# Optimization experiments

Measured on AMD Instinct MI355X. Metric: run time of the kernel, lower is better.

## Reference

```python
import jax, jax.numpy as jnp
import numpy as np

B, HOR, E, L = 16, 512, 1024, 12
ACT_NUM, DIM, ADIM = 10, 64, 10
N = 2 * HOR                      # backbone sequence length (test=False)
NPOS = 4 * (1 + HOR)             # wpe table size
D_IN = 3 + DIM * ACT_NUM + ADIM  # embed_transition input dim = 653


def setup_inputs() -> dict:
    key = jax.random.key(0)
    ks = jax.random.split(key, 12)
    s = lambda k, shape: (jax.random.normal(k, shape, jnp.float32) * 0.02)
    return {
        "action_set": jax.random.normal(ks[0], (B, ACT_NUM, DIM), jnp.float32),
        "context_rewards": jax.random.normal(ks[1], (B, HOR, 1), jnp.float32),
        "wpe": s(ks[2], (NPOS, E)),
        "W_emb": s(ks[3], (D_IN, E)),
        "b_emb": jnp.zeros((E,), jnp.float32),
        "Wq": s(ks[4], (L, E, E)),
        "Wk": s(ks[5], (L, E, E)),
        "Wv": s(ks[6], (L, E, E)),
        "ln1_g": jnp.ones((L, E), jnp.float32),
        "ln1_b": jnp.zeros((L, E), jnp.float32),
        "W1": s(ks[7], (L, E, E)),
        "b1": jnp.zeros((L, E), jnp.float32),
        "W2": s(ks[8], (L, E, E)),
        "b2": jnp.zeros((L, E), jnp.float32),
        "ln2_g": jnp.ones((L, E), jnp.float32),
        "ln2_b": jnp.zeros((L, E), jnp.float32),
        "W_pred": s(ks[9], (E, ADIM)),
        "b_pred": jnp.zeros((ADIM,), jnp.float32),
    }


def _layernorm(x, g, b, eps=1e-5):
    mu = x.mean(-1, keepdims=True)
    var = ((x - mu) ** 2).mean(-1, keepdims=True)
    return (x - mu) * jax.lax.rsqrt(var + eps) * g + b


def reference(action_set, context_rewards, wpe, W_emb, b_emb, Wq, Wk, Wv,
              ln1_g, ln1_b, W1, b1, W2, b2, ln2_g, ln2_b, W_pred, b_pred):
    batch = action_set.shape[0]
    hor = context_rewards.shape[1]
    n = 2 * hor
    # --- build interleaved sequence (outer Transformer glue) ---
    a = action_set.reshape(batch, 1, -1)                       # [B,1,DA]
    pair = jnp.concatenate([a, jnp.zeros_like(a)], axis=1)     # [B,2,DA]
    act_set_seq = jnp.tile(pair, (1, hor, 1))                  # [B,2H,DA]
    action_seq = jnp.zeros((batch, n, ADIM + 1), jnp.float32)
    one_seq = jnp.ones((batch, n, 1), jnp.float32)
    pos_seq = jnp.broadcast_to(
        jnp.arange(1, n + 1, dtype=jnp.float32).reshape(1, n, 1), (batch, n, 1))
    seq = jnp.concatenate([act_set_seq, action_seq, one_seq, pos_seq], axis=2)  # [B,N,D_IN]
    # --- DecoderTransformerBackbone ---
    Hs = seq @ W_emb + b_emb
    Hs = Hs + wpe[:n]                                          # positional embedding
    idx = jnp.arange(n)
    # normalized causal mask: row i has 1/(i+1) on j<=i, else 0
    mask = jnp.where(idx[:, None] >= idx[None, :],
                     1.0 / (idx[:, None].astype(jnp.float32) + 1.0), 0.0)
    for l in range(Wq.shape[0]):
        q = Hs @ Wq[l]
        k = Hs @ Wk[l]
        v = Hs @ Wv[l]
        attn = jax.nn.relu(jnp.einsum('bid,bjd->bij', q, k)) * mask
        Hs = Hs + jnp.einsum('bij,bjd->bid', attn, v)
        Hs = _layernorm(Hs, ln1_g[l], ln1_b[l])
        Hs = Hs + (jax.nn.relu(Hs @ W1[l] + b1[l]) @ W2[l] + b2[l])
        Hs = _layernorm(Hs, ln2_g[l], ln2_b[l])
    preds = Hs @ W_pred + b_pred                               # [B,N,ADIM]
    return preds[:, 0::2, :]                                   # [B,HOR,ADIM]
```

## Files before the change

### kernel.cpp

```cpp
#include <hip/hip_runtime.h>
#include <stdint.h>
#include <stddef.h>

#define E_DIM 1024
#define B_SZ  16
#define N_SEQ 1024
#define L_NUM 12
#define ACT_D 640
#define ADIM_ 10

typedef unsigned short u16;
typedef __attribute__((ext_vector_type(8))) short bf16x8;
typedef __attribute__((ext_vector_type(4))) float f32x4;

__device__ __forceinline__ u16 f2bf(float x) {
  union { float f; unsigned int u; } c; c.f = x;
  unsigned int r = c.u + 0x7fffu + ((c.u >> 16) & 1u);
  return (u16)(r >> 16);
}
__device__ __forceinline__ float bf2f(u16 h) {
  union { unsigned int u; float f; } c; c.u = ((unsigned int)h) << 16;
  return c.f;
}

struct us4 { u16 x, y, z, w; };

#define GLD16(gsrc, ldst) __builtin_amdgcn_global_load_lds( \
    (const __attribute__((address_space(1))) void*)(gsrc),  \
    (__attribute__((address_space(3))) void*)(ldst), 16, 0, 0)

#define BM 256
#define BK 32

template<int MODE, int EPI, int BNT>
__global__ __launch_bounds__(512)
void gemm_nt_mfma(const u16* __restrict__ Ah, const u16* __restrict__ Al,
                  const u16* __restrict__ Bh0, const u16* __restrict__ Bl0,
                  const u16* __restrict__ Bh1, const u16* __restrict__ Bl1,
                  float* __restrict__ Co,
                  u16* __restrict__ Ch0, u16* __restrict__ Cl0,
                  u16* __restrict__ Ch1, u16* __restrict__ Cl1,
                  const float* __restrict__ bias0, const float* __restrict__ bias1,
                  int K, int lda, int ldb, int ldc, int tilesN,
                  long long sA, long long sB, long long sC)
{
  constexpr int LA = BM * BK;
  constexpr int LB = BNT * BK;
  constexpr int BUFU = 2 * LA + 2 * LB;
  __shared__ u16 smem[2 * BUFU];

  constexpr int WAVE_R = (BNT == 256) ? 128 : 64;
  constexpr int WGC = BNT / 64;
  constexpr int MA = WAVE_R / 16;

  const int tid = threadIdx.x;
  const int bat = blockIdx.y;

  const u16* Bh = Bh0; const u16* Bl = Bl0;
  u16* Ch = Ch0; u16* Cl = Cl0;
  const float* bias = bias0;
  if (blockIdx.z) { Bh = Bh1; Bl = Bl1; Ch = Ch1; Cl = Cl1; bias = bias1; }

  Ah += bat * sA; Al += bat * sA;
  Bh += bat * sB; Bl += bat * sB;

  int bid;
  {
    const int nwg = gridDim.x;
    const int q = nwg >> 3, r = nwg & 7;
    const int xcd = blockIdx.x & 7, off = blockIdx.x >> 3;
    bid = ((xcd < r) ? xcd * (q + 1) : r * (q + 1) + (xcd - r) * q) + off;
  }

  int tm, tn;
  if (MODE == 1) {
    int t = bid, m = 0;
    while ((m + 1) * (m + 2) <= t) m++;
    tm = m; tn = t - m * (m + 1);
  } else {
    tm = bid / tilesN;
    tn = bid % tilesN;
  }
  int kend = K;
  if (MODE == 2) { int c = (tm + 1) * BM; kend = (c < K) ? c : K; }
  const int nk = kend / BK;

  const int ca0 = tid, ca1 = tid + 512;
  const int ra0 = ca0 >> 2, ra1 = ca1 >> 2;
  const int pa0 = ((ca0 & 3) ^ ((ra0 >> 1) & 3)) * 8;
  const int pa1 = ((ca1 & 3) ^ ((ra1 >> 1) & 3)) * 8;
  const int cb0 = tid, cb1 = tid + 512;
  const int rb0 = cb0 >> 2, rb1 = cb1 >> 2;
  const int pb0 = ((cb0 & 3) ^ ((rb0 >> 1) & 3)) * 8;
  const int pb1 = ((cb1 & 3) ^ ((rb1 >> 1) & 3)) * 8;

  const u16* gAh0 = Ah + (long long)(tm * BM + ra0) * lda + pa0;
  const u16* gAh1 = Ah + (long long)(tm * BM + ra1) * lda + pa1;
  const u16* gAl0 = Al + (long long)(tm * BM + ra0) * lda + pa0;
  const u16* gAl1 = Al + (long long)(tm * BM + ra1) * lda + pa1;
  const u16* gBh0 = Bh + (long long)(tn * BNT + rb0) * ldb + pb0;
  const u16* gBl0 = Bl + (long long)(tn * BNT + rb0) * ldb + pb0;
  const u16* gBh1 = Bh + (long long)(tn * BNT + rb1) * ldb + pb1;
  const u16* gBl1 = Bl + (long long)(tn * BNT + rb1) * ldb + pb1;
  const int oa0 = ca0 * 8, oa1 = ca1 * 8, ob0 = cb0 * 8, ob1 = cb1 * 8;

  auto stage_h0 = [&](int buf) {
    u16* base = smem + buf * BUFU;
    GLD16(gAh0, base + oa0);
    GLD16(gAh1, base + oa1);
    GLD16(gBh0, base + 2 * LA + ob0);
    if (BNT == 256) GLD16(gBh1, base + 2 * LA + ob1);
    gAh0 += BK; gAh1 += BK; gBh0 += BK;
    if (BNT == 256) gBh1 += BK;
  };
  auto stage_h1 = [&](int buf) {
    u16* base = smem + buf * BUFU;
    GLD16(gAl0, base + LA + oa0);
    GLD16(gAl1, base + LA + oa1);
    GLD16(gBl0, base + 2 * LA + LB + ob0);
    if (BNT == 256) GLD16(gBl1, base + 2 * LA + LB + ob1);
    gAl0 += BK; gAl1 += BK; gBl0 += BK;
    if (BNT == 256) gBl1 += BK;
  };

#define WAIT_HALF() do { if (BNT == 256) asm volatile("s_waitcnt vmcnt(4)" ::: "memory"); \
                         else            asm volatile("s_waitcnt vmcnt(3)" ::: "memory"); } while (0)
#define WAIT_ZERO() asm volatile("s_waitcnt vmcnt(0)" ::: "memory")
#define LGKM0()     asm volatile("s_waitcnt lgkmcnt(0)" ::: "memory")

  const int lane = tid & 63;
  const int w = tid >> 6;
  const int wr = w / WGC, wc = w % WGC;
  const int fr = lane & 15;
  const int kq = (lane >> 4) * 8;
  const int sa = ((fr >> 1) & 3) << 3;
  const int aoff = ((wr * WAVE_R + fr) * BK + kq) ^ sa;
  const int boff = ((wc * 64 + fr) * BK + kq) ^ sa;

  f32x4 acc[MA][4];
  #pragma unroll
  for (int m = 0; m < MA; m++)
    #pragma unroll
    for (int n = 0; n < 4; n++) acc[m][n] = (f32x4){0.f, 0.f, 0.f, 0.f};

  stage_h0(0);
  stage_h1(0);
  WAIT_HALF();
  __builtin_amdgcn_s_barrier();

  for (int t = 0; t < nk; t++) {
    const u16* sb = smem + (t & 1) * BUFU;
    const bool pf = (t + 1 < nk);
    const int nb = (t + 1) & 1;

    bf16x8 ah[MA], al[MA], bh[4], bl[4];

    #pragma unroll
    for (int m = 0; m < MA; m++) ah[m] = *(const bf16x8*)(sb + aoff + m * (16 * BK));
    #pragma unroll
    for (int n = 0; n < 4; n++) bh[n] = *(const bf16x8*)(sb + 2 * LA + boff + n * (16 * BK));
    if (pf) { stage_h0(nb); WAIT_HALF(); } else WAIT_ZERO();
    __builtin_amdgcn_s_barrier();
    LGKM0();
    __builtin_amdgcn_s_setprio(1);
    #pragma unroll
    for (int m = 0; m < MA; m++)
      #pragma unroll
      for (int n = 0; n < 4; n++)
        acc[m][n] = __builtin_amdgcn_mfma_f32_16x16x32_bf16(ah[m], bh[n], acc[m][n], 0, 0, 0);
    __builtin_amdgcn_s_setprio(0);
    __builtin_amdgcn_s_barrier();

    #pragma unroll
    for (int m = 0; m < MA; m++) al[m] = *(const bf16x8*)(sb + LA + aoff + m * (16 * BK));
    if (pf) stage_h1(nb);
    __builtin_amdgcn_s_barrier();
    LGKM0();
    __builtin_amdgcn_s_setprio(1);
    #pragma unroll
    for (int m = 0; m < MA; m++)
      #pragma unroll
      for (int n = 0; n < 4; n++)
        acc[m][n] = __builtin_amdgcn_mfma_f32_16x16x32_bf16(al[m], bh[n], acc[m][n], 0, 0, 0);
    __builtin_amdgcn_s_setprio(0);
    __builtin_amdgcn_s_barrier();

    #pragma unroll
    for (int n = 0; n < 4; n++) bl[n] = *(const bf16x8*)(sb + 2 * LA + LB + boff + n * (16 * BK));
    if (pf) WAIT_HALF(); else WAIT_ZERO();
    __builtin_amdgcn_s_barrier();
    LGKM0();
    __builtin_amdgcn_s_setprio(1);
    #pragma unroll
    for (int m = 0; m < MA; m++)
      #pragma unroll
      for (int n = 0; n < 4; n++)
        acc[m][n] = __builtin_amdgcn_mfma_f32_16x16x32_bf16(ah[m], bl[n], acc[m][n], 0, 0, 0);
    __builtin_amdgcn_s_setprio(0);
    __builtin_amdgcn_s_barrier();
  }

  if (Co) Co += bat * sC;
  if (Ch) { Ch += bat * sC; Cl += bat * sC; }
  #pragma unroll
  for (int m = 0; m < MA; m++) {
    #pragma unroll
    for (int r = 0; r < 4; r++) {
      const long long row = (long long)tm * BM + wr * WAVE_R + m * 16 + (lane >> 4) * 4 + r;
      #pragma unroll
      for (int n = 0; n < 4; n++) {
        const long long col = (long long)tn * BNT + wc * 64 + n * 16 + (lane & 15);
        float v = acc[m][n][r];
        if (EPI == 2) { v += bias[col]; v = v > 0.f ? v : 0.f; }
        if (EPI == 4) { v += bias[col]; }
        if (EPI == 3) {
          v = v > 0.f ? v : 0.f;
          v = (col <= row) ? v / (float)(row + 1) : 0.f;
        }
        const long long idx = row * (long long)ldc + col;
        if (EPI == 0 || EPI == 4) {
          Co[idx] = v;
        } else {
          u16 h = f2bf(v);
          Ch[idx] = h;
          Cl[idx] = f2bf(v - bf2f(h));
        }
      }
    }
  }
#undef WAIT_HALF
#undef WAIT_ZERO
#undef LGKM0
}

struct TP3 {
  const float* s0; const float* s1; const float* s2;
  u16* h0; u16* l0; u16* h1; u16* l1; u16* h2; u16* l2;
};

__global__ __launch_bounds__(256)
void transpose_split3(TP3 p)
{
  __shared__ float tile[32][33];
  const float* src; u16* dh; u16* dl;
  if (blockIdx.z == 0)      { src = p.s0; dh = p.h0; dl = p.l0; }
  else if (blockIdx.z == 1) { src = p.s1; dh = p.h1; dl = p.l1; }
  else                      { src = p.s2; dh = p.h2; dl = p.l2; }
  const int c0 = blockIdx.x * 32, r0 = blockIdx.y * 32;
  const int tx = threadIdx.x & 31, ty = threadIdx.x >> 5;
  #pragma unroll
  for (int i = ty; i < 32; i += 8)
    tile[i][tx] = src[(long long)(r0 + i) * E_DIM + c0 + tx];
  __syncthreads();
  #pragma unroll
  for (int i = ty; i < 32; i += 8) {
    const float v = tile[tx][i];
    const u16 h = f2bf(v);
    const long long idx = (long long)(c0 + i) * E_DIM + r0 + tx;
    dh[idx] = h;
    dl[idx] = f2bf(v - bf2f(h));
  }
}

__global__ __launch_bounds__(256)
void resid_ln(u16* __restrict__ hh, u16* __restrict__ hl,
              const float* __restrict__ delta,
              const float* __restrict__ g, const float* __restrict__ bta)
{
  __shared__ float red[8];
  const long long row = blockIdx.x;
  u16* hp = hh + row * E_DIM;
  u16* lp = hl + row * E_DIM;
  const float* dp = delta + row * E_DIM;
  const int tid = threadIdx.x;
  const int e = tid * 4;

  us4 hv = *(const us4*)(hp + e);
  us4 lv = *(const us4*)(lp + e);
  float4 d = *(const float4*)(dp + e);
  float x0 = bf2f(hv.x) + bf2f(lv.x) + d.x;
  float x1 = bf2f(hv.y) + bf2f(lv.y) + d.y;
  float x2 = bf2f(hv.z) + bf2f(lv.z) + d.z;
  float x3 = bf2f(hv.w) + bf2f(lv.w) + d.w;
  float s = x0 + x1 + x2 + x3;
  float q = x0 * x0 + x1 * x1 + x2 * x2 + x3 * x3;
  #pragma unroll
  for (int o = 32; o > 0; o >>= 1) { s += __shfl_down(s, o); q += __shfl_down(q, o); }
  const int lane = tid & 63, wv = tid >> 6;
  if (lane == 0) { red[wv] = s; red[wv + 4] = q; }
  __syncthreads();
  const float st = red[0] + red[1] + red[2] + red[3];
  const float qt = red[4] + red[5] + red[6] + red[7];
  const float mu = st * (1.0f / E_DIM);
  const float var = qt * (1.0f / E_DIM) - mu * mu;
  const float rstd = rsqrtf(var + 1e-5f);

  float4 gg = *(const float4*)(g + e);
  float4 bb = *(const float4*)(bta + e);
  float y0 = (x0 - mu) * rstd * gg.x + bb.x;
  float y1 = (x1 - mu) * rstd * gg.y + bb.y;
  float y2 = (x2 - mu) * rstd * gg.z + bb.z;
  float y3 = (x3 - mu) * rstd * gg.w + bb.w;

  us4 ho, lo;
  ho.x = f2bf(y0); lo.x = f2bf(y0 - bf2f(ho.x));
  ho.y = f2bf(y1); lo.y = f2bf(y1 - bf2f(ho.y));
  ho.z = f2bf(y2); lo.z = f2bf(y2 - bf2f(ho.z));
  ho.w = f2bf(y3); lo.w = f2bf(y3 - bf2f(ho.w));
  *(us4*)(hp + e) = ho;
  *(us4*)(lp + e) = lo;
}

__global__ __launch_bounds__(256)
void emb_dot(const float* __restrict__ act, const float* __restrict__ Wemb,
             float* __restrict__ Aemb)
{
  const int e = blockIdx.x * 256 + threadIdx.x;
  const int b = blockIdx.y;
  const float* ab = act + b * ACT_D;
  float s = 0.f;
  for (int d = 0; d < ACT_D; d++)
    s = fmaf(ab[d], Wemb[(long long)d * E_DIM + e], s);
  Aemb[b * E_DIM + e] = s;
}

__global__ __launch_bounds__(256)
void emb_fill(const float* __restrict__ Aemb, const float* __restrict__ Wemb,
              const float* __restrict__ bemb, const float* __restrict__ wpe,
              u16* __restrict__ oh, u16* __restrict__ ol)
{
  const int i = blockIdx.x, b = blockIdx.y;
  const int e = threadIdx.x * 4;
  float4 a;
  if ((i & 1) == 0) a = *(const float4*)(Aemb + b * E_DIM + e);
  else { a.x = 0.f; a.y = 0.f; a.z = 0.f; a.w = 0.f; }
  float4 be = *(const float4*)(bemb + e);
  float4 w1 = *(const float4*)(Wemb + 651LL * E_DIM + e);
  float4 w2 = *(const float4*)(Wemb + 652LL * E_DIM + e);
  float4 pw = *(const float4*)(wpe + (long long)i * E_DIM + e);
  const float pos = (float)(i + 1);
  float y0 = a.x + be.x + w1.x + pos * w2.x + pw.x;
  float y1 = a.y + be.y + w1.y + pos * w2.y + pw.y;
  float y2 = a.z + be.z + w1.z + pos * w2.z + pw.z;
  float y3 = a.w + be.w + w1.w + pos * w2.w + pw.w;
  const long long row = (long long)b * N_SEQ + i;

  us4 ho, lo;
  ho.x = f2bf(y0); lo.x = f2bf(y0 - bf2f(ho.x));
  ho.y = f2bf(y1); lo.y = f2bf(y1 - bf2f(ho.y));
  ho.z = f2bf(y2); lo.z = f2bf(y2 - bf2f(ho.z));
  ho.w = f2bf(y3); lo.w = f2bf(y3 - bf2f(ho.w));
  *(us4*)(oh + row * E_DIM + e) = ho;
  *(us4*)(ol + row * E_DIM + e) = lo;
}

__global__ __launch_bounds__(256)
void pred_k(const u16* __restrict__ hh, const u16* __restrict__ hl,
            const float* __restrict__ Wp, const float* __restrict__ bp,
            float* __restrict__ out)
{
  __shared__ float part[4][ADIM_];
  const int h = blockIdx.x, b = blockIdx.y;
  const long long row = (long long)b * N_SEQ + 2 * h;
  const u16* xh = hh + row * E_DIM;
  const u16* xl = hl + row * E_DIM;
  float acc[ADIM_];
  #pragma unroll
  for (int a = 0; a < ADIM_; a++) acc[a] = 0.f;
  for (int e = threadIdx.x; e < E_DIM; e += 256) {
    const float xv = bf2f(xh[e]) + bf2f(xl[e]);
    const float* wq = Wp + e * ADIM_;
    #pragma unroll
    for (int a = 0; a < ADIM_; a++) acc[a] = fmaf(xv, wq[a], acc[a]);
  }
  const int lane = threadIdx.x & 63, wv = threadIdx.x >> 6;
  #pragma unroll
  for (int a = 0; a < ADIM_; a++)
    #pragma unroll
    for (int o = 32; o > 0; o >>= 1) acc[a] += __shfl_down(acc[a], o);
  if (lane == 0)
    #pragma unroll
    for (int a = 0; a < ADIM_; a++) part[wv][a] = acc[a];
  __syncthreads();
  if (threadIdx.x < ADIM_) {
    const int a = threadIdx.x;
    out[((long long)b * (N_SEQ / 2) + h) * ADIM_ + a] =
        part[0][a] + part[1][a] + part[2][a] + part[3][a] + bp[a];
  }
}

__global__ __launch_bounds__(256)
void fill_sentinel(float* p, int n, float v)
{
  int i = blockIdx.x * 256 + threadIdx.x;
  if (i < n) p[i] = v;
}

extern "C" void kernel_launch(void* const* d_in, const int* in_sizes, int n_in,
                              void* d_out, int out_size, void* d_ws, size_t ws_size,
                              hipStream_t stream)
{
  const float* act  = (const float*)d_in[0];
  const float* wpe  = (const float*)d_in[2];
  const float* Wemb = (const float*)d_in[3];
  const float* bemb = (const float*)d_in[4];
  const float* Wq   = (const float*)d_in[5];
  const float* Wk   = (const float*)d_in[6];
  const float* Wv   = (const float*)d_in[7];
  const float* ln1g = (const float*)d_in[8];
  const float* ln1b = (const float*)d_in[9];
  const float* W1   = (const float*)d_in[10];
  const float* b1   = (const float*)d_in[11];
  const float* W2   = (const float*)d_in[12];
  const float* b2   = (const float*)d_in[13];
  const float* ln2g = (const float*)d_in[14];
  const float* ln2b = (const float*)d_in[15];
  const float* Wp   = (const float*)d_in[16];
  const float* bp   = (const float*)d_in[17];
  float* out = (float*)d_out;

  const long long sQ = (long long)N_SEQ * E_DIM;
  const long long sE = (long long)E_DIM * E_DIM;

  auto need = [&](int G) -> size_t {
    return (size_t)G * sQ * 16 + (size_t)sE * 12
         + (size_t)G * E_DIM * 4 + (size_t)(1 << 20);
  };
  int G = 16;
  while (G > 1 && need(G) > ws_size) G >>= 1;
  if (need(G) > ws_size || d_ws == nullptr || G < 8) {
    fill_sentinel<<<dim3((out_size + 255) / 256), 256, 0, stream>>>(out, out_size, 1.0e7f);
    return;
  }

  char* ws = (char*)d_ws;
  size_t off = 0;
  auto alloc = [&](size_t bytes) -> void* {
    void* p = ws + off;
    off += (bytes + 255) & ~(size_t)255;
    return p;
  };
  u16* hsh = (u16*)alloc((size_t)G * sQ * 2);
  u16* hsl = (u16*)alloc((size_t)G * sQ * 2);
  u16* qh  = (u16*)alloc((size_t)G * sQ * 2);
  u16* ql  = (u16*)alloc((size_t)G * sQ * 2);
  char* kreg = (char*)alloc((size_t)G * sQ * 4);
  u16* kh = (u16*)kreg;
  u16* kl = kh + (size_t)G * sQ;
  float* dbuf = (float*)kreg;
  u16* sh_ = (u16*)alloc((size_t)G * sQ * 2);
  u16* sl_ = (u16*)alloc((size_t)G * sQ * 2);
  u16* wAh = (u16*)alloc((size_t)sE * 2);
  u16* wAl = (u16*)alloc((size_t)sE * 2);
  u16* wBh = (u16*)alloc((size_t)sE * 2);
  u16* wBl = (u16*)alloc((size_t)sE * 2);
  u16* wCh = (u16*)alloc((size_t)sE * 2);
  u16* wCl = (u16*)alloc((size_t)sE * 2);
  float* Aemb = (float*)alloc((size_t)G * E_DIM * 4);

  const bool wide = (G >= 16);
  const int triS = 20;

  const dim3 gqk((G * N_SEQ / BM) * (E_DIM / 256), 1, 2);
  const dim3 gsq(triS, G, 1);
  const dim3 gm256((G * N_SEQ / BM) * (E_DIM / 256), 1, 1);
  const dim3 gm128((G * N_SEQ / BM) * (E_DIM / 128), 1, 1);
  const dim3 gv256((N_SEQ / BM) * (E_DIM / 256), G, 1);
  const dim3 gv128((N_SEQ / BM) * (E_DIM / 128), G, 1);

  for (int g0 = 0; g0 < B_SZ; g0 += G) {
    emb_dot<<<dim3(E_DIM / 256, G), 256, 0, stream>>>(act + (long long)g0 * ACT_D, Wemb, Aemb);
    emb_fill<<<dim3(N_SEQ, G), 256, 0, stream>>>(Aemb, Wemb, bemb, wpe, hsh, hsl);

    for (int l = 0; l < L_NUM; l++) {
      const long long wof = (long long)l * sE;
      const long long bof = (long long)l * E_DIM;

      TP3 t2 = {Wq + wof, Wk + wof, Wq + wof, wAh, wAl, wBh, wBl, wAh, wAl};
      transpose_split3<<<dim3(32, 32, 2), 256, 0, stream>>>(t2);
      gemm_nt_mfma<0, 1, 256><<<gqk, 512, 0, stream>>>(hsh, hsl, wAh, wAl, wBh, wBl,
          nullptr, qh, ql, kh, kl, nullptr, nullptr,
          E_DIM, E_DIM, E_DIM, E_DIM, E_DIM / 256, 0, 0, 0);

      TP3 t3 = {Wv + wof, W1 + wof, W2 + wof, wAh, wAl, wBh, wBl, wCh, wCl};
      transpose_split3<<<dim3(32, 32, 3), 256, 0, stream>>>(t3);

      gemm_nt_mfma<1, 3, 128><<<gsq, 512, 0, stream>>>(qh, ql, kh, kl, kh, kl,
          nullptr, sh_, sl_, sh_, sl_, nullptr, nullptr,
          E_DIM, E_DIM, E_DIM, N_SEQ, 0, sQ, sQ, sQ);

      if (wide)
        gemm_nt_mfma<0, 1, 256><<<gv256, 512, 0, stream>>>(wAh, wAl, hsh, hsl, hsh, hsl,
            nullptr, qh, ql, qh, ql, nullptr, nullptr,
            E_DIM, E_DIM, E_DIM, N_SEQ, E_DIM / 256, 0, sQ, sQ);
      else
        gemm_nt_mfma<0, 1, 128><<<gv128, 512, 0, stream>>>(wAh, wAl, hsh, hsl, hsh, hsl,
            nullptr, qh, ql, qh, ql, nullptr, nullptr,
            E_DIM, E_DIM, E_DIM, N_SEQ, E_DIM / 128, 0, sQ, sQ);

      if (wide)
        gemm_nt_mfma<2, 0, 256><<<gv256, 512, 0, stream>>>(sh_, sl_, qh, ql, qh, ql,
            dbuf, nullptr, nullptr, nullptr, nullptr, nullptr, nullptr,
            N_SEQ, N_SEQ, N_SEQ, E_DIM, E_DIM / 256, sQ, sQ, sQ);
      else
        gemm_nt_mfma<2, 0, 128><<<gv128, 512, 0, stream>>>(sh_, sl_, qh, ql, qh, ql,
            dbuf, nullptr, nullptr, nullptr, nullptr, nullptr, nullptr,
            N_SEQ, N_SEQ, N_SEQ, E_DIM, E_DIM / 128, sQ, sQ, sQ);

      resid_ln<<<dim3(G * N_SEQ), 256, 0, stream>>>(hsh, hsl, dbuf,
          ln1g + bof, ln1b + bof);

      if (wide)
        gemm_nt_mfma<0, 2, 256><<<gm256, 512, 0, stream>>>(hsh, hsl, wBh, wBl, wBh, wBl,
            nullptr, qh, ql, qh, ql, b1 + bof, b1 + bof,
            E_DIM, E_DIM, E_DIM, E_DIM, E_DIM / 256, 0, 0, 0);
      else
        gemm_nt_mfma<0, 2, 128><<<gm128, 512, 0, stream>>>(hsh, hsl, wBh, wBl, wBh, wBl,
            nullptr, qh, ql, qh, ql, b1 + bof, b1 + bof,
            E_DIM, E_DIM, E_DIM, E_DIM, E_DIM / 128, 0, 0, 0);
      if (wide)
        gemm_nt_mfma<0, 4, 256><<<gm256, 512, 0, stream>>>(qh, ql, wCh, wCl, wCh, wCl,
            dbuf, nullptr, nullptr, nullptr, nullptr, b2 + bof, b2 + bof,
            E_DIM, E_DIM, E_DIM, E_DIM, E_DIM / 256, 0, 0, 0);
      else
        gemm_nt_mfma<0, 4, 128><<<gm128, 512, 0, stream>>>(qh, ql, wCh, wCl, wCh, wCl,
            dbuf, nullptr, nullptr, nullptr, nullptr, b2 + bof, b2 + bof,
            E_DIM, E_DIM, E_DIM, E_DIM, E_DIM / 128, 0, 0, 0);

      resid_ln<<<dim3(G * N_SEQ), 256, 0, stream>>>(hsh, hsl, dbuf,
          ln2g + bof, ln2b + bof);
    }

    pred_k<<<dim3(N_SEQ / 2, G), 256, 0, stream>>>(hsh, hsl, Wp, bp,
        out + (long long)g0 * (N_SEQ / 2) * ADIM_);
  }
}
```

Measured before the change: 9.021 ms.

## Split GEMM main loop into finer interleaved load/MFMA phases for BNT=256

The bf16x3 split-precision GEMM main loop is restructured so that the A and B global-to-LDS prefetches are issued separately and spread across six smaller MFMA phases (half of the M fragments each) when BNT is 256. The aim is to interleave memory traffic with compute more finely and hide load latency behind MFMA clusters. In exchange there are more barriers per K-step and the vmcnt wait placement changes, which could add synchronisation overhead. The 128-wide path keeps three phases but moves the wait points.

```diff
diff --git a/kernel.cpp b/kernel.cpp
--- a/kernel.cpp
+++ b/kernel.cpp
@@ -104,29 +104,36 @@
   const u16* gBl1 = Bl + (long long)(tn * BNT + rb1) * ldb + pb1;
   const int oa0 = ca0 * 8, oa1 = ca1 * 8, ob0 = cb0 * 8, ob1 = cb1 * 8;
 
-  auto stage_h0 = [&](int buf) {
+  auto stA_h0 = [&](int buf) {
     u16* base = smem + buf * BUFU;
-    GLD16(gAh0, base + oa0);
-    GLD16(gAh1, base + oa1);
+    GLD16(gAh0, base + oa0); GLD16(gAh1, base + oa1);
+    gAh0 += BK; gAh1 += BK;
+  };
+  auto stB_h0 = [&](int buf) {
+    u16* base = smem + buf * BUFU;
     GLD16(gBh0, base + 2 * LA + ob0);
     if (BNT == 256) GLD16(gBh1, base + 2 * LA + ob1);
-    gAh0 += BK; gAh1 += BK; gBh0 += BK;
-    if (BNT == 256) gBh1 += BK;
+    gBh0 += BK; if (BNT == 256) gBh1 += BK;
   };
-  auto stage_h1 = [&](int buf) {
+  auto stA_h1 = [&](int buf) {
     u16* base = smem + buf * BUFU;
-    GLD16(gAl0, base + LA + oa0);
-    GLD16(gAl1, base + LA + oa1);
+    GLD16(gAl0, base + LA + oa0); GLD16(gAl1, base + LA + oa1);
+    gAl0 += BK; gAl1 += BK;
+  };
+  auto stB_h1 = [&](int buf) {
+    u16* base = smem + buf * BUFU;
     GLD16(gBl0, base + 2 * LA + LB + ob0);
     if (BNT == 256) GLD16(gBl1, base + 2 * LA + LB + ob1);
-    gAl0 += BK; gAl1 += BK; gBl0 += BK;
-    if (BNT == 256) gBl1 += BK;
+    gBl0 += BK; if (BNT == 256) gBl1 += BK;
   };
 
 #define WAIT_HALF() do { if (BNT == 256) asm volatile("s_waitcnt vmcnt(4)" ::: "memory"); \
                          else            asm volatile("s_waitcnt vmcnt(3)" ::: "memory"); } while (0)
 #define WAIT_ZERO() asm volatile("s_waitcnt vmcnt(0)" ::: "memory")
 #define LGKM0()     asm volatile("s_waitcnt lgkmcnt(0)" ::: "memory")
+#define BAR()       __builtin_amdgcn_s_barrier()
+#define PRIO1()     __builtin_amdgcn_s_setprio(1)
+#define PRIO0()     __builtin_amdgcn_s_setprio(0)
 
   const int lane = tid & 63;
   const int w = tid >> 6;
@@ -143,10 +150,10 @@
     #pragma unroll
     for (int n = 0; n < 4; n++) acc[m][n] = (f32x4){0.f, 0.f, 0.f, 0.f};
 
-  stage_h0(0);
-  stage_h1(0);
+  stA_h0(0); stB_h0(0);
+  stA_h1(0); stB_h1(0);
   WAIT_HALF();
-  __builtin_amdgcn_s_barrier();
+  BAR();
 
   for (int t = 0; t < nk; t++) {
     const u16* sb = smem + (t & 1) * BUFU;
@@ -155,49 +162,109 @@
 
     bf16x8 ah[MA], al[MA], bh[4], bl[4];
 
-    #pragma unroll
-    for (int m = 0; m < MA; m++) ah[m] = *(const bf16x8*)(sb + aoff + m * (16 * BK));
-    #pragma unroll
-    for (int n = 0; n < 4; n++) bh[n] = *(const bf16x8*)(sb + 2 * LA + boff + n * (16 * BK));
-    if (pf) { stage_h0(nb); WAIT_HALF(); } else WAIT_ZERO();
-    __builtin_amdgcn_s_barrier();
-    LGKM0();
-    __builtin_amdgcn_s_setprio(1);
-    #pragma unroll
-    for (int m = 0; m < MA; m++)
-      #pragma unroll
-      for (int n = 0; n < 4; n++)
-        acc[m][n] = __builtin_amdgcn_mfma_f32_16x16x32_bf16(ah[m], bh[n], acc[m][n], 0, 0, 0);
-    __builtin_amdgcn_s_setprio(0);
-    __builtin_amdgcn_s_barrier();
-
-    #pragma unroll
-    for (int m = 0; m < MA; m++) al[m] = *(const bf16x8*)(sb + LA + aoff + m * (16 * BK));
-    if (pf) stage_h1(nb);
-    __builtin_amdgcn_s_barrier();
-    LGKM0();
-    __builtin_amdgcn_s_setprio(1);
-    #pragma unroll
-    for (int m = 0; m < MA; m++)
-      #pragma unroll
-      for (int n = 0; n < 4; n++)
-        acc[m][n] = __builtin_amdgcn_mfma_f32_16x16x32_bf16(al[m], bh[n], acc[m][n], 0, 0, 0);
-    __builtin_amdgcn_s_setprio(0);
-    __builtin_amdgcn_s_barrier();
-
-    #pragma unroll
-    for (int n = 0; n < 4; n++) bl[n] = *(const bf16x8*)(sb + 2 * LA + LB + boff + n * (16 * BK));
-    if (pf) WAIT_HALF(); else WAIT_ZERO();
-    __builtin_amdgcn_s_barrier();
-    LGKM0();
-    __builtin_amdgcn_s_setprio(1);
-    #pragma unroll
-    for (int m = 0; m < MA; m++)
-      #pragma unroll
-      for (int n = 0; n < 4; n++)
-        acc[m][n] = __builtin_amdgcn_mfma_f32_16x16x32_bf16(ah[m], bl[n], acc[m][n], 0, 0, 0);
-    __builtin_amdgcn_s_setprio(0);
-    __builtin_amdgcn_s_barrier();
+    if (BNT == 256) {
+      #pragma unroll
+      for (int m = 0; m < 4; m++) ah[m] = *(const bf16x8*)(sb + aoff + m * 512);
+      #pragma unroll
+      for (int n = 0; n < 4; n++) bh[n] = *(const bf16x8*)(sb + 2 * LA + boff + n * 512);
+      if (pf) stA_h0(nb);
+      BAR(); LGKM0(); PRIO1();
+      #pragma unroll
+      for (int m = 0; m < 4; m++)
+        #pragma unroll
+        for (int n = 0; n < 4; n++)
+          acc[m][n] = __builtin_amdgcn_mfma_f32_16x16x32_bf16(ah[m], bh[n], acc[m][n], 0, 0, 0);
+      PRIO0(); BAR();
+
+      #pragma unroll
+      for (int m = 4; m < 8; m++) ah[m] = *(const bf16x8*)(sb + aoff + m * 512);
+      if (pf) stB_h0(nb);
+      BAR(); LGKM0(); PRIO1();
+      #pragma unroll
+      for (int m = 4; m < 8; m++)
+        #pragma unroll
+        for (int n = 0; n < 4; n++)
+          acc[m][n] = __builtin_amdgcn_mfma_f32_16x16x32_bf16(ah[m], bh[n], acc[m][n], 0, 0, 0);
+      PRIO0(); BAR();
+
+      if (pf) WAIT_HALF(); else WAIT_ZERO();
+      #pragma unroll
+      for (int m = 0; m < 4; m++) al[m] = *(const bf16x8*)(sb + LA + aoff + m * 512);
+      if (pf) stA_h1(nb);
+      BAR(); LGKM0(); PRIO1();
+      #pragma unroll
+      for (int m = 0; m < 4; m++)
+        #pragma unroll
+        for (int n = 0; n < 4; n++)
+          acc[m][n] = __builtin_amdgcn_mfma_f32_16x16x32_bf16(al[m], bh[n], acc[m][n], 0, 0, 0);
+      PRIO0(); BAR();
+
+      #pragma unroll
+      for (int m = 4; m < 8; m++) al[m] = *(const bf16x8*)(sb + LA + aoff + m * 512);
+      if (pf) stB_h1(nb);
+      BAR(); LGKM0(); PRIO1();
+      #pragma unroll
+      for (int m = 4; m < 8; m++)
+        #pragma unroll
+        for (int n = 0; n < 4; n++)
+          acc[m][n] = __builtin_amdgcn_mfma_f32_16x16x32_bf16(al[m], bh[n], acc[m][n], 0, 0, 0);
+      PRIO0(); BAR();
+
+      #pragma unroll
+      for (int n = 0; n < 4; n++) bl[n] = *(const bf16x8*)(sb + 2 * LA + LB + boff + n * 512);
+      BAR(); LGKM0(); PRIO1();
+      #pragma unroll
+      for (int m = 0; m < 4; m++)
+        #pragma unroll
+        for (int n = 0; n < 4; n++)
+          acc[m][n] = __builtin_amdgcn_mfma_f32_16x16x32_bf16(ah[m], bl[n], acc[m][n], 0, 0, 0);
+      PRIO0(); BAR();
+
+      if (pf) WAIT_HALF();
+      BAR(); PRIO1();
+      #pragma unroll
+      for (int m = 4; m < 8; m++)
+        #pragma unroll
+        for (int n = 0; n < 4; n++)
+          acc[m][n] = __builtin_amdgcn_mfma_f32_16x16x32_bf16(ah[m], bl[n], acc[m][n], 0, 0, 0);
+      PRIO0(); BAR();
+    } else {
+      #pragma unroll
+      for (int m = 0; m < MA; m++) ah[m] = *(const bf16x8*)(sb + aoff + m * 512);
+      #pragma unroll
+      for (int n = 0; n < 4; n++) bh[n] = *(const bf16x8*)(sb + 2 * LA + boff + n * 512);
+      if (pf) { stA_h0(nb); stB_h0(nb); }
+      BAR(); LGKM0(); PRIO1();
+      #pragma unroll
+      for (int m = 0; m < MA; m++)
+        #pragma unroll
+        for (int n = 0; n < 4; n++)
+          acc[m][n] = __builtin_amdgcn_mfma_f32_16x16x32_bf16(ah[m], bh[n], acc[m][n], 0, 0, 0);
+      PRIO0(); BAR();
+
+      if (pf) WAIT_HALF(); else WAIT_ZERO();
+      #pragma unroll
+      for (int m = 0; m < MA; m++) al[m] = *(const bf16x8*)(sb + LA + aoff + m * 512);
+      if (pf) { stA_h1(nb); stB_h1(nb); }
+      BAR(); LGKM0(); PRIO1();
+      #pragma unroll
+      for (int m = 0; m < MA; m++)
+        #pragma unroll
+        for (int n = 0; n < 4; n++)
+          acc[m][n] = __builtin_amdgcn_mfma_f32_16x16x32_bf16(al[m], bh[n], acc[m][n], 0, 0, 0);
+      PRIO0(); BAR();
+
+      #pragma unroll
+      for (int n = 0; n < 4; n++) bl[n] = *(const bf16x8*)(sb + 2 * LA + LB + boff + n * 512);
+      if (pf) WAIT_HALF();
+      BAR(); LGKM0(); PRIO1();
+      #pragma unroll
+      for (int m = 0; m < MA; m++)
+        #pragma unroll
+        for (int n = 0; n < 4; n++)
+          acc[m][n] = __builtin_amdgcn_mfma_f32_16x16x32_bf16(ah[m], bl[n], acc[m][n], 0, 0, 0);
+      PRIO0(); BAR();
+    }
   }
 
   if (Co) Co += bat * sC;
@@ -231,6 +298,9 @@
 #undef WAIT_HALF
 #undef WAIT_ZERO
 #undef LGKM0
+#undef BAR
+#undef PRIO1
+#undef PRIO0
 }
 
 struct TP3 {
```

New measurement: 8.939 ms. About the same (-0.9%).
